# Kernel tuning notes

Hardware: AMD Instinct MI355X
Metric: run time of the kernel (lower is better)

## Reference

```python
import jax, jax.numpy as jnp
import numpy as np

HIDDEN = 1024
HEADS = 16
HEAD_DIM = HIDDEN // HEADS


def setup_inputs() -> dict:
    key = jax.random.key(0)
    ks = jax.random.split(key, 12)
    B, S = 2, 2048
    scale = 1.0 / np.sqrt(HIDDEN)
    inp = {
        "query": jax.random.normal(ks[0], (B, S, HIDDEN), dtype=jnp.float32),
        "key": jax.random.normal(ks[1], (B, S, HIDDEN), dtype=jnp.float32),
        "value": jax.random.normal(ks[2], (B, S, HIDDEN), dtype=jnp.float32),
        "mask": jax.random.randint(ks[3], (B, 1, 1, S), 0, 2, dtype=jnp.int32),
        "Wq": jax.random.normal(ks[4], (HIDDEN, HIDDEN), dtype=jnp.float32) * scale,
        "bq": jnp.zeros((HIDDEN,), dtype=jnp.float32),
        "Wk": jax.random.normal(ks[5], (HIDDEN, HIDDEN), dtype=jnp.float32) * scale,
        "bk": jnp.zeros((HIDDEN,), dtype=jnp.float32),
        "Wv": jax.random.normal(ks[6], (HIDDEN, HIDDEN), dtype=jnp.float32) * scale,
        "bv": jnp.zeros((HIDDEN,), dtype=jnp.float32),
        "Wo": jax.random.normal(ks[7], (HIDDEN, HIDDEN), dtype=jnp.float32) * scale,
        "bo": jnp.zeros((HIDDEN,), dtype=jnp.float32),
    }
    return inp


def reference(query, key, value, mask, Wq, bq, Wk, bk, Wv, bv, Wo, bo):
    B, S, _ = query.shape
    # linear projections (x @ W + b), split heads -> [B, H, S, Dh]
    def split_heads(x):
        return x.reshape(B, -1, HEADS, HEAD_DIM).transpose(0, 2, 1, 3)

    q = split_heads(query @ Wq + bq)
    k = split_heads(key @ Wk + bk)
    v = split_heads(value @ Wv + bv)

    # scaled dot-product attention, full [B,H,S,S] scores as in original
    scores = jnp.einsum("bhqd,bhkd->bhqk", q, k) / np.sqrt(HEAD_DIM)
    scores = jnp.where(mask == 0, jnp.float32(-1e9), scores)
    weights = jax.nn.softmax(scores, axis=-1)
    x = jnp.einsum("bhqk,bhkd->bhqd", weights, v)

    # merge heads -> [B, S, hidden], output projection, then transpose(1,2)
    x = x.transpose(0, 2, 1, 3).reshape(B, -1, HIDDEN)
    out = (x @ Wo + bo).transpose(0, 2, 1)  # [B, hidden, S]
    return out
```

## Files before the change

### kernel.cpp

```cpp
#include <hip/hip_runtime.h>


typedef unsigned short ushort_t;
typedef unsigned long long ull_t;
typedef __attribute__((ext_vector_type(8))) short short8;
typedef __attribute__((ext_vector_type(4))) float f32x4;

#define S_LEN 2048
#define HID 1024
#define NH 16
#define MTOT 4096
#define KB 128
#define PERHEAD 131072
#define QSCALE 0.18033688011112042f

__device__ __forceinline__ void bsplit(float x, ushort_t& h, ushort_t& l) {
  unsigned u = __float_as_uint(x);
  unsigned hr = (u + 0x7fffu + ((u >> 16) & 1u)) >> 16;
  h = (ushort_t)hr;
  float hf = __uint_as_float(hr << 16);
  float r = x - hf;
  unsigned u2 = __float_as_uint(r);
  l = (ushort_t)((u2 + 0x7fffu + ((u2 >> 16) & 1u)) >> 16);
}

__device__ __forceinline__ void qsplit4(float v0, float v1, float v2, float v3,
                                        ull_t& hi, ull_t& lo) {
  unsigned u0 = __float_as_uint(v0), u1 = __float_as_uint(v1);
  unsigned u2 = __float_as_uint(v2), u3 = __float_as_uint(v3);
  unsigned h01 = (u0 >> 16) | (u1 & 0xffff0000u);
  unsigned h23 = (u2 >> 16) | (u3 & 0xffff0000u);
  float r0 = v0 - __uint_as_float(u0 & 0xffff0000u);
  float r1 = v1 - __uint_as_float(u1 & 0xffff0000u);
  float r2 = v2 - __uint_as_float(u2 & 0xffff0000u);
  float r3 = v3 - __uint_as_float(u3 & 0xffff0000u);
  unsigned l01, l23;
  asm("v_cvt_pk_bf16_f32 %0, %1, %2" : "=v"(l01) : "v"(r0), "v"(r1));
  asm("v_cvt_pk_bf16_f32 %0, %1, %2" : "=v"(l23) : "v"(r2), "v"(r3));
  hi = (ull_t)h01 | ((ull_t)h23 << 32);
  lo = (ull_t)l01 | ((ull_t)l23 << 32);
}

__device__ __forceinline__ void gload16(const ushort_t* g, ushort_t* l) {
  __builtin_amdgcn_global_load_lds(
      (const __attribute__((address_space(1))) unsigned int*)g,
      (__attribute__((address_space(3))) unsigned int*)l, 16, 0, 0);
}

__global__ __launch_bounds__(256) void pack_mat(const float* __restrict__ src,
                                                ushort_t* __restrict__ hi,
                                                ushort_t* __restrict__ lo,
                                                int bmode) {
  int tid = blockIdx.x * 256 + threadIdx.x;
  int r = tid & 15;
  int k8 = (tid >> 4) & (KB - 1);
  int o16 = tid >> 11;
  float v[8];
  if (bmode == 0) {
    const float* s = src + (size_t)(o16 * 16 + r) * HID + k8 * 8;
    const f32x4 f0 = *(const f32x4*)s;
    const f32x4 f1 = *(const f32x4*)(s + 4);
#pragma unroll
    for (int j = 0; j < 4; ++j) { v[j] = f0[j]; v[4 + j] = f1[j]; }
  } else {
#pragma unroll
    for (int j = 0; j < 8; ++j)
      v[j] = src[(size_t)(k8 * 8 + j) * HID + o16 * 16 + r];
  }
  short8 H, L;
#pragma unroll
  for (int j = 0; j < 8; ++j) {
    ushort_t h, l;
    bsplit(v[j], h, l);
    H[j] = (short)h;
    L[j] = (short)l;
  }
  *(short8*)(hi + (size_t)tid * 8) = H;
  *(short8*)(lo + (size_t)tid * 8) = L;
}

__global__ __launch_bounds__(256) void mask_to_float(const int* __restrict__ m,
                                                     float* __restrict__ mf) {
  int i = blockIdx.x * 256 + threadIdx.x;
  mf[i] = m[i] ? 0.f : -1e9f;
}

__global__ __launch_bounds__(256) void gemm_pack(
    const ushort_t* __restrict__ Ahi, const ushort_t* __restrict__ Alo,
    const ushort_t* __restrict__ Bhi, const ushort_t* __restrict__ Blo,
    const float* __restrict__ bias, ushort_t* __restrict__ Ohi,
    ushort_t* __restrict__ Olo, float* __restrict__ Ofp, float scale,
    int mode) {
  __shared__ ushort_t lhi[8192], llo[8192];
  const int m0 = blockIdx.y * 128;
  const int n0 = blockIdx.x * 64;
  const int lane = threadIdx.x & 63;
  const int wv = threadIdx.x >> 6;
  const int wr = wv >> 1, wc = wv & 1;
  const int l15 = lane & 15, l4 = lane >> 4;

  f32x4 acc[4][2] = {};

  size_t Ab[4], Bb[2];
#pragma unroll
  for (int mi = 0; mi < 4; ++mi)
    Ab[mi] = (size_t)((m0 >> 4) + wr * 4 + mi) * 16384 + l4 * 128 + l15 * 8;
#pragma unroll
  for (int ni = 0; ni < 2; ++ni)
    Bb[ni] = (size_t)((n0 >> 4) + wc * 2 + ni) * 16384 + l4 * 128 + l15 * 8;

#pragma unroll 2
  for (int ks = 0; ks < HID / 32; ++ks) {
    short8 ah[4], al[4], bh[2], bl[2];
#pragma unroll
    for (int mi = 0; mi < 4; ++mi) {
      ah[mi] = *(const short8*)(Ahi + Ab[mi] + ks * 512);
      al[mi] = *(const short8*)(Alo + Ab[mi] + ks * 512);
    }
#pragma unroll
    for (int ni = 0; ni < 2; ++ni) {
      bh[ni] = *(const short8*)(Bhi + Bb[ni] + ks * 512);
      bl[ni] = *(const short8*)(Blo + Bb[ni] + ks * 512);
    }
#pragma unroll
    for (int mi = 0; mi < 4; ++mi)
#pragma unroll
      for (int ni = 0; ni < 2; ++ni) {
        acc[mi][ni] = __builtin_amdgcn_mfma_f32_16x16x32_bf16(al[mi], bh[ni], acc[mi][ni], 0, 0, 0);
        acc[mi][ni] = __builtin_amdgcn_mfma_f32_16x16x32_bf16(ah[mi], bl[ni], acc[mi][ni], 0, 0, 0);
        acc[mi][ni] = __builtin_amdgcn_mfma_f32_16x16x32_bf16(ah[mi], bh[ni], acc[mi][ni], 0, 0, 0);
      }
  }

  if (mode < 2) {
#pragma unroll
    for (int mi = 0; mi < 4; ++mi)
#pragma unroll
      for (int ni = 0; ni < 2; ++ni) {
        int col = wc * 32 + ni * 16 + l15;
        float bvv = bias[n0 + col];
#pragma unroll
        for (int i = 0; i < 4; ++i) {
          int row = wr * 64 + mi * 16 + l4 * 4 + i;
          float v = (acc[mi][ni][i] + bvv) * scale;
          ushort_t hh, ll;
          bsplit(v, hh, ll);
          int loc = (mode == 0)
                        ? (((row >> 4) * 8 + (col >> 3)) * 128 + (row & 15) * 8 + (col & 7))
                        : (((col >> 4) * 16 + (row >> 3)) * 128 + (col & 15) * 8 + (row & 7));
          lhi[loc] = hh;
          llo[loc] = ll;
        }
      }
    __syncthreads();
    const int hd = n0 >> 6;
    const int b_ = m0 >> 11;
    const int s0 = m0 & (S_LEN - 1);
    const size_t hb = (size_t)(b_ * NH + hd) * PERHEAD;
#pragma unroll
    for (int r2 = 0; r2 < 2; ++r2) {
      int t = r2 * 256 + threadIdx.x;
      size_t dst;
      if (mode == 0) {
        int m16loc = (t * 16) >> 10, rem = (t * 16) & 1023;
        dst = hb + (size_t)((s0 >> 4) + m16loc) * 1024 + rem;
      } else {
        int dg = (t * 16) >> 11, rem = (t * 16) & 2047;
        dst = hb + (size_t)dg * 32768 + (size_t)(s0 >> 3) * 128 + rem;
      }
      *(short8*)(Ohi + dst) = *(const short8*)&lhi[t * 16];
      *(short8*)(Ohi + dst + 8) = *(const short8*)&lhi[t * 16 + 8];
      *(short8*)(Olo + dst) = *(const short8*)&llo[t * 16];
      *(short8*)(Olo + dst + 8) = *(const short8*)&llo[t * 16 + 8];
    }
  } else {
#pragma unroll
    for (int mi = 0; mi < 4; ++mi)
#pragma unroll
      for (int ni = 0; ni < 2; ++ni) {
        int col = n0 + wc * 32 + ni * 16 + l15;
        float bvv = bias[col];
        int m = m0 + wr * 64 + mi * 16 + l4 * 4;
        int b_ = m >> 11, s = m & (S_LEN - 1);
        f32x4 v = acc[mi][ni];
        v[0] += bvv; v[1] += bvv; v[2] += bvv; v[3] += bvv;
        *(f32x4*)(Ofp + (size_t)(b_ * HID + col) * S_LEN + s) = v;
      }
  }
}

__global__ __launch_bounds__(256) void attn_kernel(
    const ushort_t* __restrict__ Qhi, const ushort_t* __restrict__ Qlo,
    const ushort_t* __restrict__ Khi, const ushort_t* __restrict__ Klo,
    const ushort_t* __restrict__ Vhi, const ushort_t* __restrict__ Vlo,
    const float* __restrict__ maskF, ushort_t* __restrict__ Xhi,
    ushort_t* __restrict__ Xlo) {
  __shared__ ushort_t KtH[4096], KtL[4096], VtH[4096], VtL[4096];
  __shared__ ushort_t PH[4][2][1024], PL[4][2][1024];
  const int qb = blockIdx.x, h = blockIdx.y, b = blockIdx.z;
  const int lane = threadIdx.x & 63, wv = threadIdx.x >> 6;
  const int l15 = lane & 15, l4 = lane >> 4;
  const size_t hb = (size_t)(b * NH + h) * PERHEAD;

  short8 qh[2][2], ql[2][2];
#pragma unroll
  for (int qi = 0; qi < 2; ++qi)
#pragma unroll
    for (int kk = 0; kk < 2; ++kk) {
      size_t o = hb + (size_t)(qb * 8 + wv * 2 + qi) * 1024 + (kk * 4 + l4) * 128 + l15 * 8;
      qh[qi][kk] = *(const short8*)(Qhi + o);
      ql[qi][kk] = *(const short8*)(Qlo + o);
    }

  const float* mrow = maskF + b * S_LEN;
  f32x4 o_acc[2][4] = {};
  float m_r[2] = {-1e30f, -1e30f}, l_r[2] = {0.f, 0.f};

  for (int kt = 0; kt < S_LEN / 64; ++kt) {
    __syncthreads();
#pragma unroll
    for (int c = 0; c < 2; ++c) {
      int chunk = wv * 2 + c;
      size_t ko = hb + (size_t)kt * 4096 + chunk * 512 + lane * 8;
      gload16(Khi + ko, &KtH[chunk * 512]);
      gload16(Klo + ko, &KtL[chunk * 512]);
      int dg = chunk >> 1, hf = chunk & 1;
      size_t vo = hb + (size_t)dg * 32768 + (size_t)kt * 1024 + hf * 512 + lane * 8;
      gload16(Vhi + vo, &VtH[chunk * 512]);
      gload16(Vlo + vo, &VtL[chunk * 512]);
    }
    f32x4 mf[4];
#pragma unroll
    for (int cg = 0; cg < 4; ++cg)
      mf[cg] = *(const f32x4*)(mrow + kt * 64 + cg * 16 + l4 * 4);
    asm volatile("s_waitcnt vmcnt(0)" ::: "memory");
    __syncthreads();

    f32x4 sc[2][4];
#pragma unroll
    for (int cg = 0; cg < 4; ++cg) {
      short8 kh[2], kl[2];
#pragma unroll
      for (int kk = 0; kk < 2; ++kk) {
        int e = cg * 1024 + (kk * 4 + l4) * 128 + l15 * 8;
        kh[kk] = *(const short8*)&KtH[e];
        kl[kk] = *(const short8*)&KtL[e];
      }
#pragma unroll
      for (int qi = 0; qi < 2; ++qi) {
        f32x4 a = {};
#pragma unroll
        for (int kk = 0; kk < 2; ++kk) {
          a = __builtin_amdgcn_mfma_f32_16x16x32_bf16(kl[kk], qh[qi][kk], a, 0, 0, 0);
          a = __builtin_amdgcn_mfma_f32_16x16x32_bf16(kh[kk], ql[qi][kk], a, 0, 0, 0);
          a = __builtin_amdgcn_mfma_f32_16x16x32_bf16(kh[kk], qh[qi][kk], a, 0, 0, 0);
        }
        a[0] += mf[cg][0]; a[1] += mf[cg][1]; a[2] += mf[cg][2]; a[3] += mf[cg][3];
        sc[qi][cg] = a;
      }
    }

#pragma unroll
    for (int qi = 0; qi < 2; ++qi) {
      float tm = fmaxf(fmaxf(fmaxf(sc[qi][0][0], sc[qi][0][1]), fmaxf(sc[qi][0][2], sc[qi][0][3])),
                       fmaxf(fmaxf(sc[qi][1][0], sc[qi][1][1]), fmaxf(sc[qi][1][2], sc[qi][1][3])));
      float tm2 = fmaxf(fmaxf(fmaxf(sc[qi][2][0], sc[qi][2][1]), fmaxf(sc[qi][2][2], sc[qi][2][3])),
                        fmaxf(fmaxf(sc[qi][3][0], sc[qi][3][1]), fmaxf(sc[qi][3][2], sc[qi][3][3])));
      tm = fmaxf(tm, tm2);
      tm = fmaxf(tm, __shfl_xor(tm, 16));
      tm = fmaxf(tm, __shfl_xor(tm, 32));
      float mn = fmaxf(m_r[qi], tm);
      float fs = exp2f(m_r[qi] - mn);
      m_r[qi] = mn;
#pragma unroll
      for (int dg = 0; dg < 4; ++dg) o_acc[qi][dg] *= fs;
      float ts = 0.f;
#pragma unroll
      for (int cg = 0; cg < 4; ++cg) {
        float p0 = exp2f(sc[qi][cg][0] - mn);
        float p1 = exp2f(sc[qi][cg][1] - mn);
        float p2 = exp2f(sc[qi][cg][2] - mn);
        float p3 = exp2f(sc[qi][cg][3] - mn);
        ts += (p0 + p1) + (p2 + p3);
        ull_t hi, lo;
        qsplit4(p0, p1, p2, p3, hi, lo);
        int e = (cg * 2 + (l4 >> 1)) * 128 + l15 * 8 + (l4 & 1) * 4;
        *(ull_t*)&PH[wv][qi][e] = hi;
        *(ull_t*)&PL[wv][qi][e] = lo;
      }
      ts += __shfl_xor(ts, 16);
      ts += __shfl_xor(ts, 32);
      l_r[qi] = l_r[qi] * fs + ts;
    }

#pragma unroll
    for (int kk = 0; kk < 2; ++kk) {
      short8 vh[4], vl[4];
#pragma unroll
      for (int dg = 0; dg < 4; ++dg) {
        int e = dg * 1024 + (kk * 4 + l4) * 128 + l15 * 8;
        vh[dg] = *(const short8*)&VtH[e];
        vl[dg] = *(const short8*)&VtL[e];
      }
#pragma unroll
      for (int qi = 0; qi < 2; ++qi) {
        int pe = (kk * 4 + l4) * 128 + l15 * 8;
        short8 pbh = *(const short8*)&PH[wv][qi][pe];
        short8 pbl = *(const short8*)&PL[wv][qi][pe];
#pragma unroll
        for (int dg = 0; dg < 4; ++dg) {
          o_acc[qi][dg] = __builtin_amdgcn_mfma_f32_16x16x32_bf16(vh[dg], pbl, o_acc[qi][dg], 0, 0, 0);
          o_acc[qi][dg] = __builtin_amdgcn_mfma_f32_16x16x32_bf16(vl[dg], pbh, o_acc[qi][dg], 0, 0, 0);
          o_acc[qi][dg] = __builtin_amdgcn_mfma_f32_16x16x32_bf16(vh[dg], pbh, o_acc[qi][dg], 0, 0, 0);
        }
      }
    }
  }

#pragma unroll
  for (int qi = 0; qi < 2; ++qi) {
    float rl = 1.0f / l_r[qi];
    int m16 = b * 128 + qb * 8 + wv * 2 + qi;
#pragma unroll
    for (int dg = 0; dg < 4; ++dg) {
      float v0 = o_acc[qi][dg][0] * rl;
      float v1 = o_acc[qi][dg][1] * rl;
      float v2 = o_acc[qi][dg][2] * rl;
      float v3 = o_acc[qi][dg][3] * rl;
      ull_t hi, lo;
      qsplit4(v0, v1, v2, v3, hi, lo);
      size_t dst = (size_t)m16 * 16384 + (size_t)(h * 8 + dg * 2 + (l4 >> 1)) * 128 + l15 * 8 + (l4 & 1) * 4;
      *(ull_t*)(Xhi + dst) = hi;
      *(ull_t*)(Xlo + dst) = lo;
    }
  }
}

extern "C" void kernel_launch(void* const* d_in, const int* in_sizes, int n_in,
                              void* d_out, int out_size, void* d_ws,
                              size_t ws_size, hipStream_t stream) {
  (void)in_sizes; (void)n_in; (void)out_size; (void)ws_size;
  const float* query = (const float*)d_in[0];
  const float* key = (const float*)d_in[1];
  const float* value = (const float*)d_in[2];
  const int* mask = (const int*)d_in[3];
  const float* Wq = (const float*)d_in[4];
  const float* bq = (const float*)d_in[5];
  const float* Wk = (const float*)d_in[6];
  const float* bk = (const float*)d_in[7];
  const float* Wv = (const float*)d_in[8];
  const float* bv = (const float*)d_in[9];
  const float* Wo = (const float*)d_in[10];
  const float* bo = (const float*)d_in[11];
  float* out = (float*)d_out;

  const size_t EL = (size_t)MTOT * HID;
  const size_t WEL = (size_t)HID * HID;
  ushort_t* p = (ushort_t*)d_ws;
  ushort_t* X0h = p;            ushort_t* X0l = X0h + EL;
  ushort_t* X1h = X0l + EL;     ushort_t* X1l = X1h + EL;
  ushort_t* X2h = X1l + EL;     ushort_t* X2l = X2h + EL;
  ushort_t* W0h = X2l + EL;     ushort_t* W0l = W0h + WEL;
  ushort_t* W1h = W0l + WEL;    ushort_t* W1l = W1h + WEL;
  ushort_t* W2h = W1l + WEL;    ushort_t* W2l = W2h + WEL;
  ushort_t* W3h = W2l + WEL;    ushort_t* W3l = W3h + WEL;
  ushort_t* Qh = W3l + WEL;     ushort_t* Ql = Qh + EL;
  float* maskF = (float*)W0h;

  pack_mat<<<dim3(2048), dim3(256), 0, stream>>>(query, X0h, X0l, 0);
  pack_mat<<<dim3(2048), dim3(256), 0, stream>>>(key, X1h, X1l, 0);
  pack_mat<<<dim3(2048), dim3(256), 0, stream>>>(value, X2h, X2l, 0);
  pack_mat<<<dim3(512), dim3(256), 0, stream>>>(Wq, W0h, W0l, 1);
  pack_mat<<<dim3(512), dim3(256), 0, stream>>>(Wk, W1h, W1l, 1);
  pack_mat<<<dim3(512), dim3(256), 0, stream>>>(Wv, W2h, W2l, 1);
  pack_mat<<<dim3(512), dim3(256), 0, stream>>>(Wo, W3h, W3l, 1);

  dim3 gg(HID / 64, MTOT / 128);
  gemm_pack<<<gg, 256, 0, stream>>>(X0h, X0l, W0h, W0l, bq, Qh, Ql, nullptr,
                                    QSCALE, 0);
  mask_to_float<<<dim3(16), dim3(256), 0, stream>>>(mask, maskF);
  gemm_pack<<<gg, 256, 0, stream>>>(X1h, X1l, W1h, W1l, bk, X0h, X0l, nullptr,
                                    1.0f, 0);
  gemm_pack<<<gg, 256, 0, stream>>>(X2h, X2l, W2h, W2l, bv, X1h, X1l, nullptr,
                                    1.0f, 1);

  attn_kernel<<<dim3(S_LEN / 128, NH, 2), 256, 0, stream>>>(
      Qh, Ql, X0h, X0l, X1h, X1l, maskF, X2h, X2l);

  gemm_pack<<<gg, 256, 0, stream>>>(X2h, X2l, W3h, W3l, bo, nullptr, nullptr,
                                    out, 1.0f, 2);
}
```

Before: 428.0 us.

## Stage projection GEMM operands through LDS and skip redundant softmax rescaling

The projection GEMM now copies the hi/lo bf16 A and B tiles cooperatively into one shared buffer with gload16 each k-step, then reads MFMA fragments from LDS. Previously each wave fetched its fragments directly from global memory. The attention kernel skips the exp2 and the accumulator rescale when no lane's running max increases, using a wave-wide vote. The LDS staging adds two barriers and a full vmcnt wait per k-step with no double buffering, so load latency is exposed.

```diff
diff --git a/kernel.cpp b/kernel.cpp
--- a/kernel.cpp
+++ b/kernel.cpp
@@ -91,7 +91,7 @@
     const float* __restrict__ bias, ushort_t* __restrict__ Ohi,
     ushort_t* __restrict__ Olo, float* __restrict__ Ofp, float scale,
     int mode) {
-  __shared__ ushort_t lhi[8192], llo[8192];
+  __shared__ ushort_t sbuf[16384];
   const int m0 = blockIdx.y * 128;
   const int n0 = blockIdx.x * 64;
   const int lane = threadIdx.x & 63;
@@ -101,26 +101,49 @@
 
   f32x4 acc[4][2] = {};
 
-  size_t Ab[4], Bb[2];
-#pragma unroll
-  for (int mi = 0; mi < 4; ++mi)
-    Ab[mi] = (size_t)((m0 >> 4) + wr * 4 + mi) * 16384 + l4 * 128 + l15 * 8;
-#pragma unroll
-  for (int ni = 0; ni < 2; ++ni)
-    Bb[ni] = (size_t)((n0 >> 4) + wc * 2 + ni) * 16384 + l4 * 128 + l15 * 8;
-
-#pragma unroll 2
+  const ushort_t* gsrc[6];
+  ushort_t* ldst[6];
+  {
+    const size_t ab = (size_t)(m0 >> 4) * 16384 + lane * 8;
+    const size_t bb = (size_t)(n0 >> 4) * 16384 + lane * 8;
+#pragma unroll
+    for (int t = 0; t < 6; ++t) {
+      int c = t * 4 + wv;
+      if (c < 8) {
+        gsrc[t] = Ahi + ab + (size_t)c * 16384;
+        ldst[t] = &sbuf[c * 512];
+      } else if (c < 16) {
+        gsrc[t] = Alo + ab + (size_t)(c - 8) * 16384;
+        ldst[t] = &sbuf[4096 + (c - 8) * 512];
+      } else if (c < 20) {
+        gsrc[t] = Bhi + bb + (size_t)(c - 16) * 16384;
+        ldst[t] = &sbuf[8192 + (c - 16) * 512];
+      } else {
+        gsrc[t] = Blo + bb + (size_t)(c - 20) * 16384;
+        ldst[t] = &sbuf[10240 + (c - 20) * 512];
+      }
+    }
+  }
+
   for (int ks = 0; ks < HID / 32; ++ks) {
+    __syncthreads();
+#pragma unroll
+    for (int t = 0; t < 6; ++t) gload16(gsrc[t] + ks * 512, ldst[t]);
+    asm volatile("s_waitcnt vmcnt(0)" ::: "memory");
+    __syncthreads();
+
     short8 ah[4], al[4], bh[2], bl[2];
 #pragma unroll
     for (int mi = 0; mi < 4; ++mi) {
-      ah[mi] = *(const short8*)(Ahi + Ab[mi] + ks * 512);
-      al[mi] = *(const short8*)(Alo + Ab[mi] + ks * 512);
+      int e = (wr * 4 + mi) * 512 + l4 * 128 + l15 * 8;
+      ah[mi] = *(const short8*)&sbuf[e];
+      al[mi] = *(const short8*)&sbuf[4096 + e];
     }
 #pragma unroll
     for (int ni = 0; ni < 2; ++ni) {
-      bh[ni] = *(const short8*)(Bhi + Bb[ni] + ks * 512);
-      bl[ni] = *(const short8*)(Blo + Bb[ni] + ks * 512);
+      int e = (wc * 2 + ni) * 512 + l4 * 128 + l15 * 8;
+      bh[ni] = *(const short8*)&sbuf[8192 + e];
+      bl[ni] = *(const short8*)&sbuf[10240 + e];
     }
 #pragma unroll
     for (int mi = 0; mi < 4; ++mi)
@@ -133,6 +156,7 @@
   }
 
   if (mode < 2) {
+    __syncthreads();
 #pragma unroll
     for (int mi = 0; mi < 4; ++mi)
 #pragma unroll
@@ -148,8 +172,8 @@
           int loc = (mode == 0)
                         ? (((row >> 4) * 8 + (col >> 3)) * 128 + (row & 15) * 8 + (col & 7))
                         : (((col >> 4) * 16 + (row >> 3)) * 128 + (col & 15) * 8 + (row & 7));
-          lhi[loc] = hh;
-          llo[loc] = ll;
+          sbuf[loc] = hh;
+          sbuf[8192 + loc] = ll;
         }
       }
     __syncthreads();
@@ -168,10 +192,10 @@
         int dg = (t * 16) >> 11, rem = (t * 16) & 2047;
         dst = hb + (size_t)dg * 32768 + (size_t)(s0 >> 3) * 128 + rem;
       }
-      *(short8*)(Ohi + dst) = *(const short8*)&lhi[t * 16];
-      *(short8*)(Ohi + dst + 8) = *(const short8*)&lhi[t * 16 + 8];
-      *(short8*)(Olo + dst) = *(const short8*)&llo[t * 16];
-      *(short8*)(Olo + dst + 8) = *(const short8*)&llo[t * 16 + 8];
+      *(short8*)(Ohi + dst) = *(const short8*)&sbuf[t * 16];
+      *(short8*)(Ohi + dst + 8) = *(const short8*)&sbuf[t * 16 + 8];
+      *(short8*)(Olo + dst) = *(const short8*)&sbuf[8192 + t * 16];
+      *(short8*)(Olo + dst + 8) = *(const short8*)&sbuf[8192 + t * 16 + 8];
     }
   } else {
 #pragma unroll
@@ -269,11 +293,17 @@
       tm = fmaxf(tm, tm2);
       tm = fmaxf(tm, __shfl_xor(tm, 16));
       tm = fmaxf(tm, __shfl_xor(tm, 32));
-      float mn = fmaxf(m_r[qi], tm);
-      float fs = exp2f(m_r[qi] - mn);
-      m_r[qi] = mn;
-#pragma unroll
-      for (int dg = 0; dg < 4; ++dg) o_acc[qi][dg] *= fs;
+      float mn;
+      if (__all(tm <= m_r[qi])) {
+        mn = m_r[qi];
+      } else {
+        mn = fmaxf(m_r[qi], tm);
+        float fs = exp2f(m_r[qi] - mn);
+        m_r[qi] = mn;
+        l_r[qi] *= fs;
+#pragma unroll
+        for (int dg = 0; dg < 4; ++dg) o_acc[qi][dg] *= fs;
+      }
       float ts = 0.f;
 #pragma unroll
       for (int cg = 0; cg < 4; ++cg) {
@@ -290,7 +320,7 @@
       }
       ts += __shfl_xor(ts, 16);
       ts += __shfl_xor(ts, 32);
-      l_r[qi] = l_r[qi] * fs + ts;
+      l_r[qi] += ts;
     }
 
 #pragma unroll
```

Result: faster. 405.5 us (-5.3%).
